# Kernel optimization log

Hardware: AMD Instinct MI355X
Metric: run time of the kernel (lower is better)

## Reference

```python
import jax, jax.numpy as jnp
import numpy as np

B, T, M = 8, 4096, 1024
EPS = 1e-6
WINDOW = 15.0
INIT_GATE_BIAS = -3.0


def setup_inputs() -> dict:
    key = jax.random.key(0)
    k1, _ = jax.random.split(key)
    x = jax.random.normal(k1, (B, T, M), dtype=jnp.float32)
    # causal mask as in typical usage: lower-triangular (T, T)
    mask = jnp.tril(jnp.ones((T, T), dtype=jnp.float32))
    # learned gate parameter initialized to init_gate_bias
    gate_raw = jnp.full((M,), INIT_GATE_BIAS, dtype=jnp.float32)
    return {"x": x, "mask": mask, "gate_raw": gate_raw}


def _bump_kernel(T_len: int) -> jnp.ndarray:
    # K[i,j] convex bump in (i-j), supported on j in [i-window, i], K[i,i]=1
    i = jnp.arange(T_len, dtype=jnp.float32)[:, None]
    j = jnp.arange(T_len, dtype=jnp.float32)[None, :]
    diff = jnp.clip(i - j, 0.0, WINDOW)
    u = jnp.minimum(diff / WINDOW, 1.0 - EPS)
    K = jnp.exp(1.0 - 1.0 / (1.0 - u * u + EPS))
    K = jnp.where(i - j > WINDOW, 0.0, K)
    return K


def reference(x, mask, gate_raw):
    Bv, Tv, Mv = x.shape
    K = _bump_kernel(Tv).astype(x.dtype)
    K = K * mask.reshape(Tv, Tv).astype(x.dtype)
    K = K / jnp.maximum(K.sum(-1, keepdims=True), EPS)
    phi = jnp.einsum('ij,bjm->bim', K, x)  # (B, T, M)
    gate = jax.nn.softplus(gate_raw).reshape(1, 1, Mv)
    return phi * gate
```

## Files before the change

### kernel.cpp

```cpp
#include <hip/hip_runtime.h>
#include <math.h>

#define B_ 8
#define T_ 4096
#define M_ 1024
#define CT 8
#define EPSF 1e-6f

typedef float fvec4 __attribute__((ext_vector_type(4)));

__global__ __launch_bounds__(256, 2) void bump_conv_kernel(
    const float* __restrict__ x,
    const float* __restrict__ gate_raw,
    float* __restrict__ out) {
  const int chunks = T_ / CT;
  const int nwg = B_ * chunks;
  const int cpx = nwg / 8;
  const int lin = ((int)blockIdx.x % 8) * cpx + (int)blockIdx.x / 8;
  const int b     = lin / chunks;
  const int chunk = lin % chunks;
  const int t0    = chunk * CT;
  const int m     = threadIdx.x * 4;

  float w[16];
  float S = 0.0f;
#pragma unroll
  for (int d = 0; d < 16; ++d) {
    float u = fminf((float)d * (1.0f / 15.0f), 1.0f - EPSF);
    float den = 1.0f - u * u + EPSF;
    w[d] = expf(1.0f - 1.0f / den);
    S += w[d];
  }
  const float rsS = 1.0f / fmaxf(S, EPSF);

  const fvec4 graw = *(const fvec4*)(gate_raw + m);
  fvec4 g;
  g.x = fmaxf(graw.x, 0.0f) + log1pf(expf(-fabsf(graw.x)));
  g.y = fmaxf(graw.y, 0.0f) + log1pf(expf(-fabsf(graw.y)));
  g.z = fmaxf(graw.z, 0.0f) + log1pf(expf(-fabsf(graw.z)));
  g.w = fmaxf(graw.w, 0.0f) + log1pf(expf(-fabsf(graw.w)));

  const float* xb = x   + (size_t)b * T_ * M_ + m;
  float*       ob = out + (size_t)b * T_ * M_ + m;

  fvec4 v[CT + 15];
#pragma unroll
  for (int j = 0; j < CT + 15; ++j) {
    const int t = t0 - 15 + j;
    v[j] = (t >= 0) ? *(const fvec4*)(xb + (size_t)t * M_)
                    : (fvec4)(0.f);
  }

#pragma unroll
  for (int s = 0; s < CT; ++s) {
    const int t = t0 + s;

    float ax = 0.f, ay = 0.f, az = 0.f, aw = 0.f;
#pragma unroll
    for (int d = 0; d < 16; ++d) {
      const fvec4 vv = v[s + 15 - d];
      const float wd = w[d];
      ax = fmaf(wd, vv.x, ax);
      ay = fmaf(wd, vv.y, ay);
      az = fmaf(wd, vv.z, az);
      aw = fmaf(wd, vv.w, aw);
    }

    float sc = rsS;
    if (t < 15) {
      float p = 0.0f;
#pragma unroll
      for (int d = 0; d < 16; ++d) p += (d <= t) ? w[d] : 0.0f;
      sc = 1.0f / fmaxf(p, EPSF);
    }

    fvec4 o;
    o.x = ax * sc * g.x;
    o.y = ay * sc * g.y;
    o.z = az * sc * g.z;
    o.w = aw * sc * g.w;
    __builtin_nontemporal_store(o, (fvec4*)(ob + (size_t)t * M_));
  }
}

extern "C" void kernel_launch(void* const* d_in, const int* in_sizes, int n_in,
                              void* d_out, int out_size, void* d_ws, size_t ws_size,
                              hipStream_t stream) {
  const float* x         = (const float*)d_in[0];
  const float* gate_raw  = (const float*)d_in[2];
  float*       out       = (float*)d_out;

  dim3 grid(B_ * (T_ / CT));
  dim3 block(256);
  bump_conv_kernel<<<grid, block, 0, stream>>>(x, gate_raw, out);
}
```

Baseline: 263.4 us.

## Stage input rows through LDS via direct global-to-LDS loads, halve chunk size

Replaces the per-thread vector global loads of the input window with __builtin_amdgcn_global_load_lds copies into a shared buffer, then reads the rows back from LDS into registers. It also halves the time-chunk per workgroup from 8 to 4, which roughly doubles the redundant halo reads (19 rows loaded per 4 outputs) but lowers register pressure and increases the number of workgroups. The LDS footprint (~76 KB) may limit occupancy. The code waits on vmcnt only and has no barrier before the LDS reads, although each thread reads back only the slot it wrote itself.

```diff
diff --git a/kernel.cpp b/kernel.cpp
--- a/kernel.cpp
+++ b/kernel.cpp
@@ -4,15 +4,20 @@
 #define B_ 8
 #define T_ 4096
 #define M_ 1024
-#define CT 8
+#define CT 4
+#define NR (CT + 15)
 #define EPSF 1e-6f
 
 typedef float fvec4 __attribute__((ext_vector_type(4)));
+typedef const void __attribute__((address_space(1)))* gas1_t;
+typedef void       __attribute__((address_space(3)))* las3_t;
 
 __global__ __launch_bounds__(256, 2) void bump_conv_kernel(
     const float* __restrict__ x,
     const float* __restrict__ gate_raw,
     float* __restrict__ out) {
+  __shared__ float lds[NR * M_];
+
   const int chunks = T_ / CT;
   const int nwg = B_ * chunks;
   const int cpx = nwg / 8;
@@ -20,7 +25,8 @@
   const int b     = lin / chunks;
   const int chunk = lin % chunks;
   const int t0    = chunk * CT;
-  const int m     = threadIdx.x * 4;
+  const int tid   = threadIdx.x;
+  const int wid   = tid >> 6;
 
   float w[16];
   float S = 0.0f;
@@ -33,23 +39,34 @@
   }
   const float rsS = 1.0f / fmaxf(S, EPSF);
 
-  const fvec4 graw = *(const fvec4*)(gate_raw + m);
+  const fvec4 graw = *(const fvec4*)(gate_raw + tid * 4);
   fvec4 g;
   g.x = fmaxf(graw.x, 0.0f) + log1pf(expf(-fabsf(graw.x)));
   g.y = fmaxf(graw.y, 0.0f) + log1pf(expf(-fabsf(graw.y)));
   g.z = fmaxf(graw.z, 0.0f) + log1pf(expf(-fabsf(graw.z)));
   g.w = fmaxf(graw.w, 0.0f) + log1pf(expf(-fabsf(graw.w)));
 
-  const float* xb = x   + (size_t)b * T_ * M_ + m;
-  float*       ob = out + (size_t)b * T_ * M_ + m;
+  const float* xb = x   + (size_t)b * T_ * M_ + tid * 4;
+  float*       ob = out + (size_t)b * T_ * M_ + tid * 4;
 
-  fvec4 v[CT + 15];
 #pragma unroll
-  for (int j = 0; j < CT + 15; ++j) {
+  for (int j = 0; j < NR; ++j) {
     const int t = t0 - 15 + j;
-    v[j] = (t >= 0) ? *(const fvec4*)(xb + (size_t)t * M_)
-                    : (fvec4)(0.f);
+    if (t >= 0) {
+      __builtin_amdgcn_global_load_lds(
+          (gas1_t)(const void*)(xb + (size_t)t * M_),
+          (las3_t)(void*)&lds[j * M_ + wid * 256],
+          16, 0, 0);
+    } else {
+      *(fvec4*)&lds[j * M_ + tid * 4] = (fvec4)(0.f);
+    }
   }
+  asm volatile("s_waitcnt vmcnt(0)" ::: "memory");
+
+  fvec4 v[NR];
+#pragma unroll
+  for (int j = 0; j < NR; ++j)
+    v[j] = *(const fvec4*)&lds[j * M_ + tid * 4];
 
 #pragma unroll
   for (int s = 0; s < CT; ++s) {
```

Result: no change. 258.6 us (-1.9%).
